# Optimization experiments

Hardware: AMD Instinct MI355X
Metric: run time of the kernel (lower is better)

Reference implementation:

```python
import jax, jax.numpy as jnp
import numpy as np

B, S, D, H = 128, 4096, 64, 256  # num_mlps, tokens per MLP, d_model, d_hidden


def setup_inputs() -> dict:
    key = jax.random.key(0)
    kx, k1, k2 = jax.random.split(key, 3)
    x = jax.random.normal(kx, (B, S, D), dtype=jnp.float32)
    # Stacked per-MLP weights (one 2-layer SiLU MLP per batch index, no bias)
    W1 = jax.random.normal(k1, (B, D, H), dtype=jnp.float32) * (1.0 / np.sqrt(D))
    W2 = jax.random.normal(k2, (B, H, D), dtype=jnp.float32) * (1.0 / np.sqrt(H))
    return {"x": x, "W1": W1, "W2": W2}


def reference(x, W1, W2):
    # outputs[i] = mlp_i(x[i]); stacked + residual -> one batched GEMM pair
    h = jax.nn.silu(jnp.einsum('bsd,bdh->bsh', x, W1))  # [B,S,H]
    out = jnp.einsum('bsh,bhd->bsd', h, W2)             # [B,S,D]
    return out + x
```

## Files before the change

### kernel.cpp

```cpp
#include <hip/hip_runtime.h>
#include <stdint.h>

#define BB 128
#define SS 4096
#define DD 64
#define HH 256

typedef short bf16x8 __attribute__((ext_vector_type(8)));
typedef float f32x16 __attribute__((ext_vector_type(16)));

__device__ __forceinline__ uint32_t cvt_pk_bf16(float lo, float hi) {
  uint32_t r;
  asm("v_cvt_pk_bf16_f32 %0, %1, %2" : "=v"(r) : "v"(lo), "v"(hi));
  return r;
}

__device__ __forceinline__ float bflo(uint32_t w) {
  union { uint32_t u; float f; } c; c.u = w << 16; return c.f;
}
__device__ __forceinline__ float bfhi(uint32_t w) {
  union { uint32_t u; float f; } c; c.u = w & 0xffff0000u; return c.f;
}

__device__ __forceinline__ float silu_f(float v) {
  float e = __expf(-v);
  return v * __builtin_amdgcn_rcpf(1.0f + e);
}

__device__ __forceinline__ void gload16(const void* g, void* l) {
  __builtin_amdgcn_global_load_lds(
      (const __attribute__((address_space(1))) void*)g,
      (__attribute__((address_space(3))) void*)l, 16, 0, 0);
}

__global__ __launch_bounds__(256) void transpose_w(
    const float* __restrict__ W1, const float* __restrict__ W2,
    ushort* __restrict__ W1t, ushort* __restrict__ W2t) {
  int g = blockIdx.x * 256 + threadIdx.x;
  const int half = (BB * DD * HH) / 8;
  float v[8];
  if (g < half) {
    size_t e = (size_t)g * 8;
    int b = (int)(e >> 14);
    int rem = (int)(e & 16383);
    int h = rem >> 6;
    int d0 = rem & 63;
    const float* src = W1 + ((size_t)b << 14) + h;
#pragma unroll
    for (int j = 0; j < 8; ++j) v[j] = src[(size_t)(d0 + j) << 8];
    uint4 o;
    o.x = cvt_pk_bf16(v[0], v[1]); o.y = cvt_pk_bf16(v[2], v[3]);
    o.z = cvt_pk_bf16(v[4], v[5]); o.w = cvt_pk_bf16(v[6], v[7]);
    *reinterpret_cast<uint4*>(W1t + e) = o;
  } else if (g < 2 * half) {
    size_t e = (size_t)(g - half) * 8;
    int b = (int)(e >> 14);
    int rem = (int)(e & 16383);
    int d = rem >> 8;
    int h0 = rem & 255;
    const float* src = W2 + ((size_t)b << 14) + d;
#pragma unroll
    for (int j = 0; j < 8; ++j) v[j] = src[(size_t)(h0 + j) << 6];
    uint4 o;
    o.x = cvt_pk_bf16(v[0], v[1]); o.y = cvt_pk_bf16(v[2], v[3]);
    o.z = cvt_pk_bf16(v[4], v[5]); o.w = cvt_pk_bf16(v[6], v[7]);
    *reinterpret_cast<uint4*>(W2t + e) = o;
  }
}

__global__ __launch_bounds__(512, 2) void mlp_fused(
    const float* __restrict__ xg, const ushort* __restrict__ w1t,
    const ushort* __restrict__ w2t, float* __restrict__ outg) {
  __shared__ int4 lds4[131072 / 16];
  char* lds = (char*)lds4;

  const int tid = threadIdx.x;
  const int wave = tid >> 6;
  const int lane = tid & 63;
  const int l31 = lane & 31;
  const int g5 = lane >> 5;

  int raw = blockIdx.x;
  int logical = (raw & 7) * 128 + (raw >> 3);
  const int b = logical >> 3;
  const int st = logical & 7;
  const int s_base = st * 512 + wave * 64;

  const char* w1b = (const char*)(w1t + ((size_t)b << 14));
  const char* w2b = (const char*)(w2t + ((size_t)b << 14));
#pragma unroll
  for (int r = 0; r < 4; ++r) {
    uint32_t o = (uint32_t)(r * 8192 + wave * 1024 + lane * 16);
    gload16(w1b + (o ^ (((o >> 7) & 7) << 4)), lds + (r * 8192 + wave * 1024));
    gload16(w2b + (o ^ (((o >> 9) & 7) << 4)),
            lds + 32768 + (r * 8192 + wave * 1024));
  }

  char* hbase = lds + 65536 + wave * 8192;

  const float* xb = xg + (((size_t)b * SS + s_base) << 6);
#pragma unroll
  for (int it = 0; it < 8; ++it) {
    int e = it * 512 + lane * 8;
    int s = e >> 6, d0 = e & 63;
    float4 fa = *reinterpret_cast<const float4*>(xb + ((size_t)s << 6) + d0);
    float4 fb = *reinterpret_cast<const float4*>(xb + ((size_t)s << 6) + d0 + 4);
    uint4 pk;
    pk.x = cvt_pk_bf16(fa.x, fa.y); pk.y = cvt_pk_bf16(fa.z, fa.w);
    pk.z = cvt_pk_bf16(fb.x, fb.y); pk.w = cvt_pk_bf16(fb.z, fb.w);
    uint32_t byte = (uint32_t)(s * 128 + d0 * 2);
    byte ^= (uint32_t)(s & 7) << 4;
    *reinterpret_cast<uint4*>(hbase + byte) = pk;
  }

  bf16x8 bx[2][4];
#pragma unroll
  for (int nt = 0; nt < 2; ++nt)
#pragma unroll
    for (int kc = 0; kc < 4; ++kc) {
      int s = nt * 32 + l31;
      uint32_t byte = (uint32_t)(s * 128 + kc * 32 + g5 * 16);
      byte ^= (uint32_t)(s & 7) << 4;
      bx[nt][kc] = *reinterpret_cast<const bf16x8*>(hbase + byte);
    }

  f32x16 acc[2][2];
#pragma unroll
  for (int mt = 0; mt < 2; ++mt)
#pragma unroll
    for (int nt = 0; nt < 2; ++nt) {
      int s = nt * 32 + l31;
      uint32_t sw = (uint32_t)(s & 7) << 4;
#pragma unroll
      for (int q = 0; q < 4; ++q) {
        uint32_t byte = (uint32_t)(s * 128 + mt * 64 + q * 16 + g5 * 8);
        byte ^= sw;
        uint2 w = *reinterpret_cast<const uint2*>(hbase + byte);
        acc[mt][nt][4 * q + 0] = bflo(w.x);
        acc[mt][nt][4 * q + 1] = bfhi(w.x);
        acc[mt][nt][4 * q + 2] = bflo(w.y);
        acc[mt][nt][4 * q + 3] = bfhi(w.y);
      }
    }
  __builtin_amdgcn_sched_barrier(0);
  __syncthreads();

  const f32x16 vzero = {0.f, 0.f, 0.f, 0.f, 0.f, 0.f, 0.f, 0.f,
                        0.f, 0.f, 0.f, 0.f, 0.f, 0.f, 0.f, 0.f};

#pragma unroll
  for (int hb = 0; hb < 4; ++hb) {
    bf16x8 a1[2][4];
#pragma unroll
    for (int mt = 0; mt < 2; ++mt)
#pragma unroll
      for (int kc = 0; kc < 4; ++kc) {
        int hrow = hb * 64 + mt * 32 + l31;
        uint32_t byte = (uint32_t)hrow * 128 + (uint32_t)(kc * 32 + g5 * 16);
        byte ^= (uint32_t)(hrow & 7) << 4;
        a1[mt][kc] = *reinterpret_cast<const bf16x8*>(lds + byte);
      }
    f32x16 ah[2][2];
    ah[0][0] = vzero; ah[0][1] = vzero; ah[1][0] = vzero; ah[1][1] = vzero;
#pragma unroll
    for (int kc = 0; kc < 4; ++kc)
#pragma unroll
      for (int mt = 0; mt < 2; ++mt)
#pragma unroll
        for (int nt = 0; nt < 2; ++nt)
          ah[mt][nt] = __builtin_amdgcn_mfma_f32_32x32x16_bf16(
              a1[mt][kc], bx[nt][kc], ah[mt][nt], 0, 0, 0);

#pragma unroll
    for (int mt = 0; mt < 2; ++mt)
#pragma unroll
      for (int nt = 0; nt < 2; ++nt) {
        int s_loc = nt * 32 + l31;
        uint32_t sw = (uint32_t)(s_loc & 7) << 4;
#pragma unroll
        for (int q = 0; q < 4; ++q) {
          float t0 = silu_f(ah[mt][nt][4 * q + 0]);
          float t1 = silu_f(ah[mt][nt][4 * q + 1]);
          float t2 = silu_f(ah[mt][nt][4 * q + 2]);
          float t3 = silu_f(ah[mt][nt][4 * q + 3]);
          uint32_t p0 = cvt_pk_bf16(t0, t1);
          uint32_t p1 = cvt_pk_bf16(t2, t3);
          uint32_t byte =
              (uint32_t)s_loc * 128 + (uint32_t)(mt * 64 + q * 16 + g5 * 8);
          byte ^= sw;
          *reinterpret_cast<uint2*>(hbase + byte) = make_uint2(p0, p1);
        }
      }

    bf16x8 a2[2][4], bh[2][4];
#pragma unroll
    for (int mt = 0; mt < 2; ++mt)
#pragma unroll
      for (int kc = 0; kc < 4; ++kc) {
        int drow = mt * 32 + l31;
        uint32_t byte = (uint32_t)drow * 512 +
                        (uint32_t)(hb * 128 + kc * 32 + g5 * 16);
        byte ^= (uint32_t)(drow & 7) << 4;
        a2[mt][kc] = *reinterpret_cast<const bf16x8*>(lds + 32768 + byte);
      }
#pragma unroll
    for (int nt = 0; nt < 2; ++nt)
#pragma unroll
      for (int kc = 0; kc < 4; ++kc) {
        int s_loc = nt * 32 + l31;
        uint32_t byte = (uint32_t)s_loc * 128 + (uint32_t)(kc * 32 + g5 * 16);
        byte ^= (uint32_t)(s_loc & 7) << 4;
        bh[nt][kc] = *reinterpret_cast<const bf16x8*>(hbase + byte);
      }
#pragma unroll
    for (int kc = 0; kc < 4; ++kc)
#pragma unroll
      for (int mt = 0; mt < 2; ++mt)
#pragma unroll
        for (int nt = 0; nt < 2; ++nt)
          acc[mt][nt] = __builtin_amdgcn_mfma_f32_32x32x16_bf16(
              a2[mt][kc], bh[nt][kc], acc[mt][nt], 0, 0, 0);
  }

#pragma unroll
  for (int nt = 0; nt < 2; ++nt) {
    int s_loc = l31;
    uint32_t sw = (uint32_t)(s_loc & 7) << 4;
#pragma unroll
    for (int mt = 0; mt < 2; ++mt)
#pragma unroll
      for (int q = 0; q < 4; ++q) {
        uint32_t byte =
            (uint32_t)s_loc * 256 + (uint32_t)(mt * 128 + q * 32 + g5 * 16);
        byte ^= sw;
        float4 v;
        v.x = acc[mt][nt][4 * q + 0];
        v.y = acc[mt][nt][4 * q + 1];
        v.z = acc[mt][nt][4 * q + 2];
        v.w = acc[mt][nt][4 * q + 3];
        *reinterpret_cast<float4*>(hbase + byte) = v;
      }
    __builtin_amdgcn_sched_barrier(0);
#pragma unroll
    for (int it = 0; it < 8; ++it) {
      uint32_t o = (uint32_t)(it * 1024 + lane * 16);
      uint32_t row = o >> 8;
      uint32_t byte = o ^ ((row & 7) << 4);
      float4 v = *reinterpret_cast<const float4*>(hbase + byte);
      size_t s = (size_t)s_base + nt * 32 + row;
      size_t goff = (((size_t)b * SS + s) << 6) + ((o & 255) >> 2);
      *reinterpret_cast<float4*>(outg + goff) = v;
    }
    __builtin_amdgcn_sched_barrier(0);
  }
}

extern "C" void kernel_launch(void* const* d_in, const int* in_sizes, int n_in,
                              void* d_out, int out_size, void* d_ws, size_t ws_size,
                              hipStream_t stream) {
  const float* x  = (const float*)d_in[0];
  const float* W1 = (const float*)d_in[1];
  const float* W2 = (const float*)d_in[2];
  float* out = (float*)d_out;

  ushort* W1t = (ushort*)d_ws;
  ushort* W2t = W1t + (size_t)BB * DD * HH;

  transpose_w<<<2048, 256, 0, stream>>>(W1, W2, W1t, W2t);
  mlp_fused<<<1024, 512, 0, stream>>>(x, W1t, W2t, out);
}
```

Measured before the change: 98.52 us.

## Keep hidden activations in registers via permlane32 swap instead of LDS round-trip

Builds the second GEMM's B operand directly from the first GEMM's accumulator registers. It uses v_permlane32_swap to rearrange bf16-packed SiLU outputs into the MFMA input layout, which removes the per-wave LDS write/read of the hidden tile. The x tile and the residual are now loaded straight from global memory into registers instead of being staged through LDS. This halves LDS usage to 64KB, which may raise occupancy. A barrier is added before the epilogue reuses the weight LDS region. In exchange, x is read from global twice and the residual is now added in fp32 rather than after bf16 rounding.

```diff
diff --git a/kernel.cpp b/kernel.cpp
--- a/kernel.cpp
+++ b/kernel.cpp
@@ -15,11 +15,8 @@
   return r;
 }
 
-__device__ __forceinline__ float bflo(uint32_t w) {
-  union { uint32_t u; float f; } c; c.u = w << 16; return c.f;
-}
-__device__ __forceinline__ float bfhi(uint32_t w) {
-  union { uint32_t u; float f; } c; c.u = w & 0xffff0000u; return c.f;
+__device__ __forceinline__ void permswap(uint32_t& a, uint32_t& b) {
+  asm("v_permlane32_swap_b32 %0, %1" : "+v"(a), "+v"(b));
 }
 
 __device__ __forceinline__ float silu_f(float v) {
@@ -71,7 +68,7 @@
 __global__ __launch_bounds__(512, 2) void mlp_fused(
     const float* __restrict__ xg, const ushort* __restrict__ w1t,
     const ushort* __restrict__ w2t, float* __restrict__ outg) {
-  __shared__ int4 lds4[131072 / 16];
+  __shared__ int4 lds4[65536 / 16];
   char* lds = (char*)lds4;
 
   const int tid = threadIdx.x;
@@ -96,32 +93,21 @@
             lds + 32768 + (r * 8192 + wave * 1024));
   }
 
-  char* hbase = lds + 65536 + wave * 8192;
-
   const float* xb = xg + (((size_t)b * SS + s_base) << 6);
-#pragma unroll
-  for (int it = 0; it < 8; ++it) {
-    int e = it * 512 + lane * 8;
-    int s = e >> 6, d0 = e & 63;
-    float4 fa = *reinterpret_cast<const float4*>(xb + ((size_t)s << 6) + d0);
-    float4 fb = *reinterpret_cast<const float4*>(xb + ((size_t)s << 6) + d0 + 4);
-    uint4 pk;
-    pk.x = cvt_pk_bf16(fa.x, fa.y); pk.y = cvt_pk_bf16(fa.z, fa.w);
-    pk.z = cvt_pk_bf16(fb.x, fb.y); pk.w = cvt_pk_bf16(fb.z, fb.w);
-    uint32_t byte = (uint32_t)(s * 128 + d0 * 2);
-    byte ^= (uint32_t)(s & 7) << 4;
-    *reinterpret_cast<uint4*>(hbase + byte) = pk;
-  }
-
   bf16x8 bx[2][4];
 #pragma unroll
   for (int nt = 0; nt < 2; ++nt)
 #pragma unroll
     for (int kc = 0; kc < 4; ++kc) {
-      int s = nt * 32 + l31;
-      uint32_t byte = (uint32_t)(s * 128 + kc * 32 + g5 * 16);
-      byte ^= (uint32_t)(s & 7) << 4;
-      bx[nt][kc] = *reinterpret_cast<const bf16x8*>(hbase + byte);
+      const float* p = xb + ((size_t)(nt * 32 + l31) << 6) + kc * 16 + g5 * 8;
+      float4 fa = *reinterpret_cast<const float4*>(p);
+      float4 fb = *reinterpret_cast<const float4*>(p + 4);
+      union { uint32_t u[4]; bf16x8 v; } cv;
+      cv.u[0] = cvt_pk_bf16(fa.x, fa.y);
+      cv.u[1] = cvt_pk_bf16(fa.z, fa.w);
+      cv.u[2] = cvt_pk_bf16(fb.x, fb.y);
+      cv.u[3] = cvt_pk_bf16(fb.z, fb.w);
+      bx[nt][kc] = cv.v;
     }
 
   f32x16 acc[2][2];
@@ -129,20 +115,17 @@
   for (int mt = 0; mt < 2; ++mt)
 #pragma unroll
     for (int nt = 0; nt < 2; ++nt) {
-      int s = nt * 32 + l31;
-      uint32_t sw = (uint32_t)(s & 7) << 4;
+      const float* prow = xb + ((size_t)(nt * 32 + l31) << 6);
 #pragma unroll
       for (int q = 0; q < 4; ++q) {
-        uint32_t byte = (uint32_t)(s * 128 + mt * 64 + q * 16 + g5 * 8);
-        byte ^= sw;
-        uint2 w = *reinterpret_cast<const uint2*>(hbase + byte);
-        acc[mt][nt][4 * q + 0] = bflo(w.x);
-        acc[mt][nt][4 * q + 1] = bfhi(w.x);
-        acc[mt][nt][4 * q + 2] = bflo(w.y);
-        acc[mt][nt][4 * q + 3] = bfhi(w.y);
+        float4 v = *reinterpret_cast<const float4*>(prow + mt * 32 + q * 8 + g5 * 4);
+        acc[mt][nt][4 * q + 0] = v.x;
+        acc[mt][nt][4 * q + 1] = v.y;
+        acc[mt][nt][4 * q + 2] = v.z;
+        acc[mt][nt][4 * q + 3] = v.w;
       }
     }
-  __builtin_amdgcn_sched_barrier(0);
+
   __syncthreads();
 
   const f32x16 vzero = {0.f, 0.f, 0.f, 0.f, 0.f, 0.f, 0.f, 0.f,
@@ -171,28 +154,29 @@
           ah[mt][nt] = __builtin_amdgcn_mfma_f32_32x32x16_bf16(
               a1[mt][kc], bx[nt][kc], ah[mt][nt], 0, 0, 0);
 
-#pragma unroll
-    for (int mt = 0; mt < 2; ++mt)
-#pragma unroll
-      for (int nt = 0; nt < 2; ++nt) {
-        int s_loc = nt * 32 + l31;
-        uint32_t sw = (uint32_t)(s_loc & 7) << 4;
-#pragma unroll
-        for (int q = 0; q < 4; ++q) {
-          float t0 = silu_f(ah[mt][nt][4 * q + 0]);
-          float t1 = silu_f(ah[mt][nt][4 * q + 1]);
-          float t2 = silu_f(ah[mt][nt][4 * q + 2]);
-          float t3 = silu_f(ah[mt][nt][4 * q + 3]);
-          uint32_t p0 = cvt_pk_bf16(t0, t1);
-          uint32_t p1 = cvt_pk_bf16(t2, t3);
-          uint32_t byte =
-              (uint32_t)s_loc * 128 + (uint32_t)(mt * 64 + q * 16 + g5 * 8);
-          byte ^= sw;
-          *reinterpret_cast<uint2*>(hbase + byte) = make_uint2(p0, p1);
+    bf16x8 bh[2][4];
+#pragma unroll
+    for (int nt = 0; nt < 2; ++nt)
+#pragma unroll
+      for (int mt = 0; mt < 2; ++mt)
+#pragma unroll
+        for (int c = 0; c < 2; ++c) {
+          uint32_t A0 = cvt_pk_bf16(silu_f(ah[mt][nt][8 * c + 0]),
+                                    silu_f(ah[mt][nt][8 * c + 1]));
+          uint32_t A1 = cvt_pk_bf16(silu_f(ah[mt][nt][8 * c + 2]),
+                                    silu_f(ah[mt][nt][8 * c + 3]));
+          uint32_t B0 = cvt_pk_bf16(silu_f(ah[mt][nt][8 * c + 4]),
+                                    silu_f(ah[mt][nt][8 * c + 5]));
+          uint32_t B1 = cvt_pk_bf16(silu_f(ah[mt][nt][8 * c + 6]),
+                                    silu_f(ah[mt][nt][8 * c + 7]));
+          permswap(A0, B0);
+          permswap(A1, B1);
+          union { uint32_t u[4]; bf16x8 v; } f;
+          f.u[0] = A0; f.u[1] = A1; f.u[2] = B0; f.u[3] = B1;
+          bh[nt][2 * mt + c] = f.v;
         }
-      }
-
-    bf16x8 a2[2][4], bh[2][4];
+
+    bf16x8 a2[2][4];
 #pragma unroll
     for (int mt = 0; mt < 2; ++mt)
 #pragma unroll
@@ -204,15 +188,6 @@
         a2[mt][kc] = *reinterpret_cast<const bf16x8*>(lds + 32768 + byte);
       }
 #pragma unroll
-    for (int nt = 0; nt < 2; ++nt)
-#pragma unroll
-      for (int kc = 0; kc < 4; ++kc) {
-        int s_loc = nt * 32 + l31;
-        uint32_t byte = (uint32_t)s_loc * 128 + (uint32_t)(kc * 32 + g5 * 16);
-        byte ^= (uint32_t)(s_loc & 7) << 4;
-        bh[nt][kc] = *reinterpret_cast<const bf16x8*>(hbase + byte);
-      }
-#pragma unroll
     for (int kc = 0; kc < 4; ++kc)
 #pragma unroll
       for (int mt = 0; mt < 2; ++mt)
@@ -222,6 +197,8 @@
               a2[mt][kc], bh[nt][kc], acc[mt][nt], 0, 0, 0);
   }
 
+  __syncthreads();
+  char* hbase = lds + wave * 8192;
 #pragma unroll
   for (int nt = 0; nt < 2; ++nt) {
     int s_loc = l31;
```

New measurement: 117.2 us. 19.0% more time.
